# Kernel optimization log

Measured on AMD Instinct MI355X. Metric: run time of the kernel, lower is better.

## Reference

```python
import jax, jax.numpy as jnp
import numpy as np

B, S, D, H = 4, 2048, 512, 8
DK = D // H


def setup_inputs() -> dict:
    key = jax.random.key(0)
    ks = jax.random.split(key, 11)
    scale = 1.0 / np.sqrt(D)
    inp = {
        'q': jax.random.normal(ks[0], (B, S, D), jnp.float32),
        'k': jax.random.normal(ks[1], (B, S, D), jnp.float32),
        'v': jax.random.normal(ks[2], (B, S, D), jnp.float32),
        'mask': jnp.tril(jnp.ones((S, S), jnp.int32))[None, None, :, :],  # [1,1,S,S] causal
        'w_q': jax.random.normal(ks[3], (D, D), jnp.float32) * scale,
        'b_q': jnp.zeros((D,), jnp.float32),
        'w_k': jax.random.normal(ks[4], (D, D), jnp.float32) * scale,
        'b_k': jnp.zeros((D,), jnp.float32),
        'w_v': jax.random.normal(ks[5], (D, D), jnp.float32) * scale,
        'b_v': jnp.zeros((D,), jnp.float32),
        'w_o': jax.random.normal(ks[6], (D, D), jnp.float32) * scale,
        'b_o': jnp.zeros((D,), jnp.float32),
    }
    return inp


def reference(q, k, v, mask, w_q, b_q, w_k, b_k, w_v, b_v, w_o, b_o):
    # QKV projections (nn.Linear: x @ W^T + b)
    def split_heads(x):  # [B,S,D] -> [B,H,S,DK]
        return x.reshape(B, S, H, DK).transpose(0, 2, 1, 3)

    qh = split_heads(q @ w_q.T + b_q)
    kh = split_heads(k @ w_k.T + b_k)
    vh = split_heads(v @ w_v.T + b_v)

    scores = jnp.einsum('bhqd,bhkd->bhqk', qh, kh) / jnp.sqrt(jnp.float32(DK))
    scores = jnp.where(mask == 0, jnp.float32(-1e9), scores)
    attn = jax.nn.softmax(scores, axis=-1)  # dropout is identity in eval
    ctx = jnp.einsum('bhqk,bhkd->bhqd', attn, vh)  # [B,H,S,DK]
    ctx = ctx.transpose(0, 2, 1, 3).reshape(B, S, D)
    return ctx @ w_o.T + b_o
```

## Files before the change

### kernel.cpp

```cpp
#include <hip/hip_runtime.h>
#include <hip/hip_bf16.h>


#define BATCH  4
#define SLEN   2048
#define DMODEL 512
#define NHEAD  8
#define DHEAD  64
#define MROWS  (BATCH * SLEN)

#define NQ ((size_t)MROWS * DMODEL)
#define NW ((size_t)DMODEL * DMODEL)
#define NB ((size_t)DMODEL)
#define CVT_TOTAL (3 * NQ + 4 * NW + 4 * NB)

typedef short bf16x8 __attribute__((ext_vector_type(8)));
typedef float f32x4  __attribute__((ext_vector_type(4)));

typedef unsigned int __attribute__((address_space(1))) glb_u32_t;
typedef unsigned int __attribute__((address_space(3))) lds_u32_t;

__device__ __forceinline__ void async_copy16(const unsigned short* g, unsigned short* l) {
    __builtin_amdgcn_global_load_lds((glb_u32_t*)g, (lds_u32_t*)l, 16, 0, 0);
}

__device__ __forceinline__ float bf2f(unsigned short u) {
    union { unsigned int i; float f; } v; v.i = ((unsigned int)u) << 16; return v.f;
}
__device__ __forceinline__ unsigned short f2bf(float f) {
    union { float f; unsigned int i; } v; v.f = f;
    unsigned int x = v.i;
    return (unsigned short)((x + 0x7fffu + ((x >> 16) & 1u)) >> 16);
}
__device__ __forceinline__ unsigned int pkbf(float a, float b) {
    union { __hip_bfloat162 h; unsigned int u; } cv;
    cv.h = __float22bfloat162_rn(float2{a, b});
    return cv.u;
}

__device__ __forceinline__ void barrier_lgkm() {
    asm volatile("s_waitcnt lgkmcnt(0)" ::: "memory");
    __builtin_amdgcn_s_barrier();
    asm volatile("" ::: "memory");
}

__global__ __launch_bounds__(256)
void cvt_kernel(const float* __restrict__ q, const float* __restrict__ k,
                const float* __restrict__ v,
                const float* __restrict__ wq, const float* __restrict__ wk,
                const float* __restrict__ wv, const float* __restrict__ wo,
                const float* __restrict__ bq, const float* __restrict__ bk,
                const float* __restrict__ bv, const float* __restrict__ bo,
                unsigned short* __restrict__ dst)
{
    const size_t i4 = ((size_t)blockIdx.x * 256 + threadIdx.x) * 4;
    if (i4 >= CVT_TOTAL) return;
    const float* src;
    size_t off;
    if      (i4 <     NQ)          { src = q;  off = i4; }
    else if (i4 < 2 * NQ)          { src = k;  off = i4 - NQ; }
    else if (i4 < 3 * NQ)          { src = v;  off = i4 - 2 * NQ; }
    else if (i4 < 3 * NQ + NW)     { src = wq; off = i4 - 3 * NQ; }
    else if (i4 < 3 * NQ + 2 * NW) { src = wk; off = i4 - 3 * NQ - NW; }
    else if (i4 < 3 * NQ + 3 * NW) { src = wv; off = i4 - 3 * NQ - 2 * NW; }
    else if (i4 < 3 * NQ + 4 * NW) { src = wo; off = i4 - 3 * NQ - 3 * NW; }
    else if (i4 < 3 * NQ + 4 * NW + NB)     { src = bq; off = i4 - 3 * NQ - 4 * NW; }
    else if (i4 < 3 * NQ + 4 * NW + 2 * NB) { src = bk; off = i4 - 3 * NQ - 4 * NW - NB; }
    else if (i4 < 3 * NQ + 4 * NW + 3 * NB) { src = bv; off = i4 - 3 * NQ - 4 * NW - 2 * NB; }
    else                                    { src = bo; off = i4 - 3 * NQ - 4 * NW - 3 * NB; }
    const float4 f = *(const float4*)(src + off);
    ushort4 o;
    o.x = f2bf(f.x); o.y = f2bf(f.y); o.z = f2bf(f.z); o.w = f2bf(f.w);
    *(ushort4*)(dst + i4) = o;
}

template <typename OutT>
__device__ __forceinline__ void gemm_body(const unsigned short* __restrict__ A,
                                          const unsigned short* __restrict__ W,
                                          const unsigned short* __restrict__ bias,
                                          OutT* __restrict__ C)
{
    __shared__ __align__(16) unsigned short As[2][128 * 32];
    __shared__ __align__(16) unsigned short Bs[2][128 * 32];

    const int tid  = threadIdx.x;
    const int wave = tid >> 6;
    const int lane = tid & 63;
    const int l15  = lane & 15;
    const int quad = lane >> 4;
    const int m0   = blockIdx.x * 128;
    const int n0   = blockIdx.y * 128;
    const int wm   = (wave & 1) * 64;
    const int wn   = (wave >> 1) * 64;
    const int srow = lane >> 2;
    const int scol = (((lane & 3) ^ (srow & 3)) * 8);
    const int rsw  = (quad ^ (l15 & 3)) * 8;

    auto stage = [&](int k0, int buf) {
        async_copy16(A + (size_t)(m0 + wave * 16 + srow) * DMODEL + k0 + scol, As[buf] + wave * 512);
        async_copy16(A + (size_t)(m0 + (wave + 4) * 16 + srow) * DMODEL + k0 + scol, As[buf] + (wave + 4) * 512);
        async_copy16(W + (size_t)(n0 + wave * 16 + srow) * DMODEL + k0 + scol, Bs[buf] + wave * 512);
        async_copy16(W + (size_t)(n0 + (wave + 4) * 16 + srow) * DMODEL + k0 + scol, Bs[buf] + (wave + 4) * 512);
    };

    f32x4 acc[4][4] = {};
    stage(0, 0);

    #pragma unroll 1
    for (int kt = 0; kt < 16; kt++) {
        const int cur = kt & 1, nxt = cur ^ 1;
        stage(((kt + 1) & 15) * 32, nxt);
        asm volatile("s_waitcnt vmcnt(4)" ::: "memory");
        __builtin_amdgcn_s_barrier();
        asm volatile("" ::: "memory");

        bf16x8 af[4], bfr[4];
        #pragma unroll
        for (int i = 0; i < 4; i++)
            af[i] = *(const bf16x8*)(As[cur] + (wm + i * 16 + l15) * 32 + rsw);
        #pragma unroll
        for (int j = 0; j < 4; j++)
            bfr[j] = *(const bf16x8*)(Bs[cur] + (wn + j * 16 + l15) * 32 + rsw);
        #pragma unroll
        for (int i = 0; i < 4; i++)
            #pragma unroll
            for (int j = 0; j < 4; j++)
                acc[i][j] = __builtin_amdgcn_mfma_f32_16x16x32_bf16(af[i], bfr[j], acc[i][j], 0, 0, 0);

        barrier_lgkm();
    }

    #pragma unroll
    for (int j = 0; j < 4; j++) {
        const int col = n0 + wn + j * 16 + l15;
        const float bv = bf2f(bias[col]);
        #pragma unroll
        for (int i = 0; i < 4; i++) {
            const int row = m0 + wm + i * 16 + quad * 4;
            #pragma unroll
            for (int r = 0; r < 4; r++) {
                const float val = acc[i][j][r] + bv;
                if constexpr (sizeof(OutT) == 4)
                    C[(size_t)(row + r) * DMODEL + col] = val;
                else
                    C[(size_t)(row + r) * DMODEL + col] = f2bf(val);
            }
        }
    }
}

__global__ __launch_bounds__(256, 2)
void qkv_gemm_kernel(const unsigned short* __restrict__ qin,
                     const unsigned short* __restrict__ kin,
                     const unsigned short* __restrict__ vin,
                     const unsigned short* __restrict__ wq,
                     const unsigned short* __restrict__ bq,
                     const unsigned short* __restrict__ wk,
                     const unsigned short* __restrict__ bk,
                     const unsigned short* __restrict__ wv,
                     const unsigned short* __restrict__ bv,
                     unsigned short* __restrict__ qh,
                     unsigned short* __restrict__ kh,
                     unsigned short* __restrict__ vh)
{
    const int z = blockIdx.z;
    const unsigned short* A    = (z == 0) ? qin : (z == 1) ? kin : vin;
    const unsigned short* W    = (z == 0) ? wq  : (z == 1) ? wk  : wv;
    const unsigned short* bias = (z == 0) ? bq  : (z == 1) ? bk  : bv;
    unsigned short*       C    = (z == 0) ? qh  : (z == 1) ? kh  : vh;
    gemm_body<unsigned short>(A, W, bias, C);
}

__global__ __launch_bounds__(256, 2)
void oproj_gemm_kernel(const unsigned short* __restrict__ ctx,
                       const unsigned short* __restrict__ wo,
                       const unsigned short* __restrict__ bo,
                       float* __restrict__ out)
{
    gemm_body<float>(ctx, wo, bo, out);
}

#define VT_STRIDE 72
#define PS_STRIDE 72
#define SCALE_L2E 0.180336880f

__global__ __launch_bounds__(256, 2)
void attn_kernel(const unsigned short* __restrict__ qh,
                 const unsigned short* __restrict__ kh,
                 const unsigned short* __restrict__ vh,
                 unsigned short* __restrict__ ctx)
{
    __shared__ __align__(16) unsigned short Ks[2][64 * 64];
    __shared__ __align__(16) unsigned short Vt[64 * VT_STRIDE];
    __shared__ __align__(16) unsigned short Ps[4 * 16 * PS_STRIDE];

    const int tid  = threadIdx.x;
    const int wave = tid >> 6;
    const int lane = tid & 63;
    const int l15  = lane & 15;
    const int quad = lane >> 4;

    const int x  = blockIdx.x;
    const int bh = blockIdx.y;
    const int b  = bh >> 3;
    const int h  = bh & 7;

    const size_t base = (size_t)b * SLEN * DMODEL + (size_t)h * DHEAD;
    const unsigned short* Q = qh + base;
    const unsigned short* K = kh + base;
    const unsigned short* V = vh + base;

    const int krow_l = lane >> 3;
    const int kcol_l = ((lane & 7) ^ (krow_l & 7)) * 8;

    int qtc  = x;
    int qrow = qtc * 64 + wave * 16 + l15;
    bf16x8 qf0 = *(const bf16x8*)(Q + (size_t)qrow * DMODEL + quad * 8);
    bf16x8 qf1 = *(const bf16x8*)(Q + (size_t)qrow * DMODEL + 32 + quad * 8);

    f32x4 oacc[4] = {};
    float m_i = -1e30f, l_i = 0.0f;

    unsigned short* Pw = Ps + wave * (16 * PS_STRIDE);
    const int itA   = x;
    const int total = 33;

    async_copy16(K + (size_t)(wave * 8 + krow_l) * DMODEL + kcol_l, Ks[0] + wave * 512);
    async_copy16(K + (size_t)((wave + 4) * 8 + krow_l) * DMODEL + kcol_l, Ks[0] + (wave + 4) * 512);
    bf16x8 v8c0 = *(const bf16x8*)(V + (size_t)lane * DMODEL + wave * 8);
    bf16x8 v8c1 = *(const bf16x8*)(V + (size_t)lane * DMODEL + wave * 8 + 32);
    bf16x8 v8n0, v8n1;

    #pragma unroll 1
    for (int it = 0; it < total; it++) {
        const int cur = it & 1, nxt = cur ^ 1;
        const int kt  = (it <= itA) ? it : it - itA - 1;
        const int itn = (it < total - 1) ? it + 1 : it;
        const int ktn = (itn <= itA) ? itn : itn - itA - 1;

        async_copy16(K + (size_t)(ktn * 64 + wave * 8 + krow_l) * DMODEL + kcol_l,
                     Ks[nxt] + wave * 512);
        async_copy16(K + (size_t)(ktn * 64 + (wave + 4) * 8 + krow_l) * DMODEL + kcol_l,
                     Ks[nxt] + (wave + 4) * 512);
        v8n0 = *(const bf16x8*)(V + (size_t)(ktn * 64 + lane) * DMODEL + wave * 8);
        v8n1 = *(const bf16x8*)(V + (size_t)(ktn * 64 + lane) * DMODEL + wave * 8 + 32);

        #pragma unroll
        for (int d = 0; d < 8; d++)
            Vt[(wave * 8 + d) * VT_STRIDE + lane] = (unsigned short)v8c0[d];
        #pragma unroll
        for (int d = 0; d < 8; d++)
            Vt[(wave * 8 + 32 + d) * VT_STRIDE + lane] = (unsigned short)v8c1[d];
        barrier_lgkm();

        f32x4 sacc[4] = {};
        #pragma unroll
        for (int kk = 0; kk < 2; kk++) {
            const bf16x8 qf = kk ? qf1 : qf0;
            #pragma unroll
            for (int j = 0; j < 4; j++) {
                bf16x8 kf = *(const bf16x8*)(Ks[cur] + (j * 16 + l15) * 64
                                                + (((kk * 4 + quad) ^ (l15 & 7)) * 8));
                sacc[j] = __builtin_amdgcn_mfma_f32_16x16x32_bf16(kf, qf, sacc[j], 0, 0, 0);
            }
        }

        const bool need_mask = (kt == qtc);
        #pragma unroll
        for (int j = 0; j < 4; j++) {
            #pragma unroll
            for (int r = 0; r < 4; r++) {
                float s = sacc[j][r] * SCALE_L2E;
                if (need_mask) {
                    const int kv = kt * 64 + j * 16 + quad * 4 + r;
                    if (kv > qrow) s = -1e30f;
                }
                sacc[j][r] = s;
            }
        }

        float mx = -1e30f;
        #pragma unroll
        for (int j = 0; j < 4; j++)
            #pragma unroll
            for (int r = 0; r < 4; r++)
                mx = fmaxf(mx, sacc[j][r]);
        mx = fmaxf(mx, __shfl_xor(mx, 16, 64));
        mx = fmaxf(mx, __shfl_xor(mx, 32, 64));
        const float mnew  = fmaxf(m_i, mx);
        const float alpha = exp2f(m_i - mnew);
        float rsum = 0.0f;
        #pragma unroll
        for (int j = 0; j < 4; j++)
            #pragma unroll
            for (int r = 0; r < 4; r++) {
                const float p = exp2f(sacc[j][r] - mnew);
                sacc[j][r] = p;
                rsum += p;
            }
        rsum += __shfl_xor(rsum, 16, 64);
        rsum += __shfl_xor(rsum, 32, 64);
        l_i = l_i * alpha + rsum;
        m_i = mnew;
        #pragma unroll
        for (int jd = 0; jd < 4; jd++)
            #pragma unroll
            for (int r = 0; r < 4; r++)
                oacc[jd][r] *= alpha;

        #pragma unroll
        for (int j = 0; j < 4; j++) {
            uint2 p2;
            p2.x = pkbf(sacc[j][0], sacc[j][1]);
            p2.y = pkbf(sacc[j][2], sacc[j][3]);
            *(uint2*)(Pw + l15 * PS_STRIDE + j * 16 + quad * 4) = p2;
        }
        asm volatile("s_waitcnt lgkmcnt(0)" ::: "memory");

        #pragma unroll
        for (int kk = 0; kk < 2; kk++) {
            bf16x8 pf = *(const bf16x8*)(Pw + l15 * PS_STRIDE + kk * 32 + quad * 8);
            #pragma unroll
            for (int jd = 0; jd < 4; jd++) {
                bf16x8 vf = *(const bf16x8*)(Vt + (jd * 16 + l15) * VT_STRIDE + kk * 32 + quad * 8);
                oacc[jd] = __builtin_amdgcn_mfma_f32_16x16x32_bf16(vf, pf, oacc[jd], 0, 0, 0);
            }
        }

        barrier_lgkm();

        if (it == itA) {
            const float invl = 1.0f / l_i;
            #pragma unroll
            for (int jd = 0; jd < 4; jd++) {
                uint2 o2;
                o2.x = pkbf(oacc[jd][0] * invl, oacc[jd][1] * invl);
                o2.y = pkbf(oacc[jd][2] * invl, oacc[jd][3] * invl);
                *(uint2*)(ctx + base + (size_t)qrow * DMODEL + jd * 16 + quad * 4) = o2;
                oacc[jd] = f32x4{0.f, 0.f, 0.f, 0.f};
            }
            m_i = -1e30f; l_i = 0.0f;
            qtc  = 31 - x;
            qrow = qtc * 64 + wave * 16 + l15;
            qf0 = *(const bf16x8*)(Q + (size_t)qrow * DMODEL + quad * 8);
            qf1 = *(const bf16x8*)(Q + (size_t)qrow * DMODEL + 32 + quad * 8);
        }
        v8c0 = v8n0; v8c1 = v8n1;
    }

    const float invl = 1.0f / l_i;
    #pragma unroll
    for (int jd = 0; jd < 4; jd++) {
        uint2 o2;
        o2.x = pkbf(oacc[jd][0] * invl, oacc[jd][1] * invl);
        o2.y = pkbf(oacc[jd][2] * invl, oacc[jd][3] * invl);
        *(uint2*)(ctx + base + (size_t)qrow * DMODEL + jd * 16 + quad * 4) = o2;
    }
}

extern "C" void kernel_launch(void* const* d_in, const int* in_sizes, int n_in,
                              void* d_out, int out_size, void* d_ws, size_t ws_size,
                              hipStream_t stream)
{
    const float* q   = (const float*)d_in[0];
    const float* k   = (const float*)d_in[1];
    const float* v   = (const float*)d_in[2];
    const float* w_q = (const float*)d_in[4];
    const float* b_q = (const float*)d_in[5];
    const float* w_k = (const float*)d_in[6];
    const float* b_k = (const float*)d_in[7];
    const float* w_v = (const float*)d_in[8];
    const float* b_v = (const float*)d_in[9];
    const float* w_o = (const float*)d_in[10];
    const float* b_o = (const float*)d_in[11];
    float* out = (float*)d_out;

    unsigned short* ws = (unsigned short*)d_ws;
    unsigned short* qb  = ws;
    unsigned short* kb  = ws + NQ;
    unsigned short* vb  = ws + 2 * NQ;
    unsigned short* wqb = ws + 3 * NQ;
    unsigned short* wkb = wqb + NW;
    unsigned short* wvb = wkb + NW;
    unsigned short* wob = wvb + NW;
    unsigned short* bqb = wob + NW;
    unsigned short* bkb = bqb + NB;
    unsigned short* bvb = bkb + NB;
    unsigned short* bob = bvb + NB;
    unsigned short* qh  = bob + NB;
    unsigned short* kh  = qh + NQ;
    unsigned short* vh  = kh + NQ;
    unsigned short* ctx = vh + NQ;

    dim3 blk(256);
    hipLaunchKernelGGL(cvt_kernel, dim3((unsigned)(CVT_TOTAL / 4 / 256)), blk, 0, stream,
                       q, k, v, w_q, w_k, w_v, w_o, b_q, b_k, b_v, b_o, ws);
    hipLaunchKernelGGL(qkv_gemm_kernel, dim3(MROWS / 128, DMODEL / 128, 3), blk, 0, stream,
                       qb, kb, vb, wqb, bqb, wkb, bkb, wvb, bvb, qh, kh, vh);
    hipLaunchKernelGGL(attn_kernel, dim3(16, BATCH * NHEAD), blk, 0, stream,
                       qh, kh, vh, ctx);
    hipLaunchKernelGGL(oproj_gemm_kernel, dim3(MROWS / 128, DMODEL / 128), blk, 0, stream,
                       ctx, wob, bob, out);
}
```

Before: 224.7 us.

## Emit transposed V from QKV GEMM, fold softmax scale into Q, one query tile per block

The QKV GEMM now writes V in a per-head transposed [b,h,dk,s] layout and pre-multiplies Q by the softmax scale times log2(e). The attention kernel can then stream both K and V^T into double-buffered LDS with async copies, instead of transposing V through registers every iteration. Attention also moves from paired query tiles (x and 31-x) to one query tile per block across a 32x32 grid, interleaving heavy and light tiles. The P buffer gets an XOR swizzle in place of padding, and launch bounds are raised. The costs are more blocks with uneven causal work, and strided 8-byte stores for the transposed V write.

```diff
diff --git a/kernel.cpp b/kernel.cpp
--- a/kernel.cpp
+++ b/kernel.cpp
@@ -13,6 +13,8 @@
 #define NW ((size_t)DMODEL * DMODEL)
 #define NB ((size_t)DMODEL)
 #define CVT_TOTAL (3 * NQ + 4 * NW + 4 * NB)
+
+#define SCALE_L2E 0.180336880f
 
 typedef short bf16x8 __attribute__((ext_vector_type(8)));
 typedef float f32x4  __attribute__((ext_vector_type(4)));
@@ -78,7 +80,7 @@
 __device__ __forceinline__ void gemm_body(const unsigned short* __restrict__ A,
                                           const unsigned short* __restrict__ W,
                                           const unsigned short* __restrict__ bias,
-                                          OutT* __restrict__ C)
+                                          OutT* __restrict__ C, int mode)
 {
     __shared__ __align__(16) unsigned short As[2][128 * 32];
     __shared__ __align__(16) unsigned short Bs[2][128 * 32];
@@ -130,26 +132,45 @@
         barrier_lgkm();
     }
 
-    #pragma unroll
-    for (int j = 0; j < 4; j++) {
-        const int col = n0 + wn + j * 16 + l15;
-        const float bv = bf2f(bias[col]);
-        #pragma unroll
-        for (int i = 0; i < 4; i++) {
-            const int row = m0 + wm + i * 16 + quad * 4;
-            #pragma unroll
-            for (int r = 0; r < 4; r++) {
-                const float val = acc[i][j][r] + bv;
-                if constexpr (sizeof(OutT) == 4)
-                    C[(size_t)(row + r) * DMODEL + col] = val;
-                else
-                    C[(size_t)(row + r) * DMODEL + col] = f2bf(val);
+    if (mode == 2) {
+        #pragma unroll
+        for (int j = 0; j < 4; j++) {
+            const int col = n0 + wn + j * 16 + l15;
+            const float bv = bf2f(bias[col]);
+            const int hh = col >> 6, dk = col & 63;
+            #pragma unroll
+            for (int i = 0; i < 4; i++) {
+                const int row = m0 + wm + i * 16 + quad * 4;
+                const int bb = row >> 11, s = row & 2047;
+                uint2 o2;
+                o2.x = pkbf(acc[i][j][0] + bv, acc[i][j][1] + bv);
+                o2.y = pkbf(acc[i][j][2] + bv, acc[i][j][3] + bv);
+                *(uint2*)((unsigned short*)C + ((size_t)((bb * NHEAD + hh) * DHEAD + dk)) * SLEN + s) = o2;
+            }
+        }
+    } else {
+        const float oscale = (mode == 0) ? SCALE_L2E : 1.0f;
+        #pragma unroll
+        for (int j = 0; j < 4; j++) {
+            const int col = n0 + wn + j * 16 + l15;
+            const float bv = bf2f(bias[col]);
+            #pragma unroll
+            for (int i = 0; i < 4; i++) {
+                const int row = m0 + wm + i * 16 + quad * 4;
+                #pragma unroll
+                for (int r = 0; r < 4; r++) {
+                    const float val = (acc[i][j][r] + bv) * oscale;
+                    if constexpr (sizeof(OutT) == 4)
+                        C[(size_t)(row + r) * DMODEL + col] = val;
+                    else
+                        C[(size_t)(row + r) * DMODEL + col] = f2bf(val);
+                }
             }
         }
     }
 }
 
-__global__ __launch_bounds__(256, 2)
+__global__ __launch_bounds__(256, 3)
 void qkv_gemm_kernel(const unsigned short* __restrict__ qin,
                      const unsigned short* __restrict__ kin,
                      const unsigned short* __restrict__ vin,
@@ -161,38 +182,34 @@
                      const unsigned short* __restrict__ bv,
                      unsigned short* __restrict__ qh,
                      unsigned short* __restrict__ kh,
-                     unsigned short* __restrict__ vh)
+                     unsigned short* __restrict__ vt)
 {
     const int z = blockIdx.z;
     const unsigned short* A    = (z == 0) ? qin : (z == 1) ? kin : vin;
     const unsigned short* W    = (z == 0) ? wq  : (z == 1) ? wk  : wv;
     const unsigned short* bias = (z == 0) ? bq  : (z == 1) ? bk  : bv;
-    unsigned short*       C    = (z == 0) ? qh  : (z == 1) ? kh  : vh;
-    gemm_body<unsigned short>(A, W, bias, C);
-}
-
-__global__ __launch_bounds__(256, 2)
+    unsigned short*       C    = (z == 0) ? qh  : (z == 1) ? kh  : vt;
+    gemm_body<unsigned short>(A, W, bias, C, z);
+}
+
+__global__ __launch_bounds__(256, 3)
 void oproj_gemm_kernel(const unsigned short* __restrict__ ctx,
                        const unsigned short* __restrict__ wo,
                        const unsigned short* __restrict__ bo,
                        float* __restrict__ out)
 {
-    gemm_body<float>(ctx, wo, bo, out);
-}
-
-#define VT_STRIDE 72
-#define PS_STRIDE 72
-#define SCALE_L2E 0.180336880f
-
-__global__ __launch_bounds__(256, 2)
+    gemm_body<float>(ctx, wo, bo, out, 3);
+}
+
+__global__ __launch_bounds__(256, 4)
 void attn_kernel(const unsigned short* __restrict__ qh,
                  const unsigned short* __restrict__ kh,
-                 const unsigned short* __restrict__ vh,
+                 const unsigned short* __restrict__ vt,
                  unsigned short* __restrict__ ctx)
 {
     __shared__ __align__(16) unsigned short Ks[2][64 * 64];
-    __shared__ __align__(16) unsigned short Vt[64 * VT_STRIDE];
-    __shared__ __align__(16) unsigned short Ps[4 * 16 * PS_STRIDE];
+    __shared__ __align__(16) unsigned short Vs[2][64 * 64];
+    __shared__ __align__(16) unsigned short Ps[4 * 16 * 64];
 
     const int tid  = threadIdx.x;
     const int wave = tid >> 6;
@@ -200,58 +217,51 @@
     const int l15  = lane & 15;
     const int quad = lane >> 4;
 
-    const int x  = blockIdx.x;
-    const int bh = blockIdx.y;
+    const int bh = blockIdx.x;
+    const int x  = blockIdx.y;
+    const int qt = (x & 1) ? (x >> 1) : (31 - (x >> 1));
     const int b  = bh >> 3;
     const int h  = bh & 7;
 
     const size_t base = (size_t)b * SLEN * DMODEL + (size_t)h * DHEAD;
-    const unsigned short* Q = qh + base;
-    const unsigned short* K = kh + base;
-    const unsigned short* V = vh + base;
+    const unsigned short* Q  = qh + base;
+    const unsigned short* K  = kh + base;
+    const unsigned short* VT = vt + (size_t)bh * DHEAD * SLEN;
 
     const int krow_l = lane >> 3;
     const int kcol_l = ((lane & 7) ^ (krow_l & 7)) * 8;
 
-    int qtc  = x;
-    int qrow = qtc * 64 + wave * 16 + l15;
+    const int qrow = qt * 64 + wave * 16 + l15;
     bf16x8 qf0 = *(const bf16x8*)(Q + (size_t)qrow * DMODEL + quad * 8);
     bf16x8 qf1 = *(const bf16x8*)(Q + (size_t)qrow * DMODEL + 32 + quad * 8);
 
     f32x4 oacc[4] = {};
     float m_i = -1e30f, l_i = 0.0f;
 
-    unsigned short* Pw = Ps + wave * (16 * PS_STRIDE);
-    const int itA   = x;
-    const int total = 33;
-
-    async_copy16(K + (size_t)(wave * 8 + krow_l) * DMODEL + kcol_l, Ks[0] + wave * 512);
-    async_copy16(K + (size_t)((wave + 4) * 8 + krow_l) * DMODEL + kcol_l, Ks[0] + (wave + 4) * 512);
-    bf16x8 v8c0 = *(const bf16x8*)(V + (size_t)lane * DMODEL + wave * 8);
-    bf16x8 v8c1 = *(const bf16x8*)(V + (size_t)lane * DMODEL + wave * 8 + 32);
-    bf16x8 v8n0, v8n1;
+    unsigned short* Pw = Ps + wave * (16 * 64);
+    const int ktiles = qt + 1;
+
+    auto stageKV = [&](int kt, int buf) {
+        async_copy16(K + (size_t)(kt * 64 + wave * 8 + krow_l) * DMODEL + kcol_l,
+                     Ks[buf] + wave * 512);
+        async_copy16(K + (size_t)(kt * 64 + (wave + 4) * 8 + krow_l) * DMODEL + kcol_l,
+                     Ks[buf] + (wave + 4) * 512);
+        async_copy16(VT + (size_t)(wave * 8 + krow_l) * SLEN + kt * 64 + kcol_l,
+                     Vs[buf] + wave * 512);
+        async_copy16(VT + (size_t)((wave + 4) * 8 + krow_l) * SLEN + kt * 64 + kcol_l,
+                     Vs[buf] + (wave + 4) * 512);
+    };
+
+    stageKV(0, 0);
 
     #pragma unroll 1
-    for (int it = 0; it < total; it++) {
-        const int cur = it & 1, nxt = cur ^ 1;
-        const int kt  = (it <= itA) ? it : it - itA - 1;
-        const int itn = (it < total - 1) ? it + 1 : it;
-        const int ktn = (itn <= itA) ? itn : itn - itA - 1;
-
-        async_copy16(K + (size_t)(ktn * 64 + wave * 8 + krow_l) * DMODEL + kcol_l,
-                     Ks[nxt] + wave * 512);
-        async_copy16(K + (size_t)(ktn * 64 + (wave + 4) * 8 + krow_l) * DMODEL + kcol_l,
-                     Ks[nxt] + (wave + 4) * 512);
-        v8n0 = *(const bf16x8*)(V + (size_t)(ktn * 64 + lane) * DMODEL + wave * 8);
-        v8n1 = *(const bf16x8*)(V + (size_t)(ktn * 64 + lane) * DMODEL + wave * 8 + 32);
-
-        #pragma unroll
-        for (int d = 0; d < 8; d++)
-            Vt[(wave * 8 + d) * VT_STRIDE + lane] = (unsigned short)v8c0[d];
-        #pragma unroll
-        for (int d = 0; d < 8; d++)
-            Vt[(wave * 8 + 32 + d) * VT_STRIDE + lane] = (unsigned short)v8c1[d];
-        barrier_lgkm();
+    for (int kt = 0; kt < ktiles; kt++) {
+        const int cur = kt & 1, nxt = cur ^ 1;
+        const int ktn = (kt + 1 < ktiles) ? kt + 1 : kt;
+        stageKV(ktn, nxt);
+        asm volatile("s_waitcnt vmcnt(4)" ::: "memory");
+        __builtin_amdgcn_s_barrier();
+        asm volatile("" ::: "memory");
 
         f32x4 sacc[4] = {};
         #pragma unroll
@@ -265,18 +275,14 @@
             }
         }
 
-        const bool need_mask = (kt == qtc);
-        #pragma unroll
-        for (int j = 0; j < 4; j++) {
-            #pragma unroll
-            for (int r = 0; r < 4; r++) {
-                float s = sacc[j][r] * SCALE_L2E;
-                if (need_mask) {
+        if (kt == qt) {
+            #pragma unroll
+            for (int j = 0; j < 4; j++)
+                #pragma unroll
+                for (int r = 0; r < 4; r++) {
                     const int kv = kt * 64 + j * 16 + quad * 4 + r;
-                    if (kv > qrow) s = -1e30f;
+                    if (kv > qrow) sacc[j][r] = -1e30f;
                 }
-                sacc[j][r] = s;
-            }
         }
 
         float mx = -1e30f;
@@ -313,40 +319,26 @@
             uint2 p2;
             p2.x = pkbf(sacc[j][0], sacc[j][1]);
             p2.y = pkbf(sacc[j][2], sacc[j][3]);
-            *(uint2*)(Pw + l15 * PS_STRIDE + j * 16 + quad * 4) = p2;
+            const int chunk = (j * 2 + (quad >> 1)) ^ (l15 & 7);
+            *(uint2*)(Pw + l15 * 64 + chunk * 8 + (quad & 1) * 4) = p2;
         }
         asm volatile("s_waitcnt lgkmcnt(0)" ::: "memory");
 
         #pragma unroll
         for (int kk = 0; kk < 2; kk++) {
-            bf16x8 pf = *(const bf16x8*)(Pw + l15 * PS_STRIDE + kk * 32 + quad * 8);
+            bf16x8 pf = *(const bf16x8*)(Pw + l15 * 64 + (((kk * 4 + quad) ^ (l15 & 7)) * 8));
             #pragma unroll
             for (int jd = 0; jd < 4; jd++) {
-                bf16x8 vf = *(const bf16x8*)(Vt + (jd * 16 + l15) * VT_STRIDE + kk * 32 + quad * 8);
+                bf16x8 vf = *(const bf16x8*)(Vs[cur] + (jd * 16 + l15) * 64
+                                                + (((kk * 4 + quad) ^ (l15 & 7)) * 8));
                 oacc[jd] = __builtin_amdgcn_mfma_f32_16x16x32_bf16(vf, pf, oacc[jd], 0, 0, 0);
             }
         }
 
         barrier_lgkm();
-
-        if (it == itA) {
-            const float invl = 1.0f / l_i;
-            #pragma unroll
-            for (int jd = 0; jd < 4; jd++) {
-                uint2 o2;
-                o2.x = pkbf(oacc[jd][0] * invl, oacc[jd][1] * invl);
-                o2.y = pkbf(oacc[jd][2] * invl, oacc[jd][3] * invl);
-                *(uint2*)(ctx + base + (size_t)qrow * DMODEL + jd * 16 + quad * 4) = o2;
-                oacc[jd] = f32x4{0.f, 0.f, 0.f, 0.f};
-            }
-            m_i = -1e30f; l_i = 0.0f;
-            qtc  = 31 - x;
-            qrow = qtc * 64 + wave * 16 + l15;
-            qf0 = *(const bf16x8*)(Q + (size_t)qrow * DMODEL + quad * 8);
-            qf1 = *(const bf16x8*)(Q + (size_t)qrow * DMODEL + 32 + quad * 8);
-        }
-        v8c0 = v8n0; v8c1 = v8n1;
     }
+
+    asm volatile("s_waitcnt vmcnt(0)" ::: "memory");
 
     const float invl = 1.0f / l_i;
     #pragma unroll
@@ -389,16 +381,16 @@
     unsigned short* bob = bvb + NB;
     unsigned short* qh  = bob + NB;
     unsigned short* kh  = qh + NQ;
-    unsigned short* vh  = kh + NQ;
-    unsigned short* ctx = vh + NQ;
+    unsigned short* vt  = kh + NQ;
+    unsigned short* ctx = vt + NQ;
 
     dim3 blk(256);
     hipLaunchKernelGGL(cvt_kernel, dim3((unsigned)(CVT_TOTAL / 4 / 256)), blk, 0, stream,
                        q, k, v, w_q, w_k, w_v, w_o, b_q, b_k, b_v, b_o, ws);
     hipLaunchKernelGGL(qkv_gemm_kernel, dim3(MROWS / 128, DMODEL / 128, 3), blk, 0, stream,
-                       qb, kb, vb, wqb, bqb, wkb, bkb, wvb, bvb, qh, kh, vh);
-    hipLaunchKernelGGL(attn_kernel, dim3(16, BATCH * NHEAD), blk, 0, stream,
-                       qh, kh, vh, ctx);
+                       qb, kb, vb, wqb, bqb, wkb, bkb, wvb, bvb, qh, kh, vt);
+    hipLaunchKernelGGL(attn_kernel, dim3(BATCH * NHEAD, 32), blk, 0, stream,
+                       qh, kh, vt, ctx);
     hipLaunchKernelGGL(oproj_gemm_kernel, dim3(MROWS / 128, DMODEL / 128), blk, 0, stream,
                        ctx, wob, bob, out);
 }
```

Result: faster. 217.1 us (-3.4%).
